# Kernel tuning notes

Measured on AMD Instinct MI355X. Metric: run time of the kernel, lower is better.

The kernel has to match this reference:

```python
import jax, jax.numpy as jnp
import numpy as np

EPS = 1e-8  # torch F.cosine_similarity norm clamp


def setup_inputs() -> dict:
    key = jax.random.key(0)
    k1, k2, k3, k4, k5 = jax.random.split(key, 5)
    C, S, H = 20000, 32, 256
    Cs = S // 2  # compressed_seq_len = int(S * 0.5)
    B = 64
    return {
        "query": jax.random.normal(k1, (B, H), dtype=jnp.float32),
        "episodes": jax.random.normal(k2, (C, S, H), dtype=jnp.float32),
        "compressed_episodes": jax.random.normal(k3, (C, Cs, H), dtype=jnp.float32),
        "episode_embeddings": jax.random.normal(k4, (C, H), dtype=jnp.float32),
        "is_compressed": jax.random.randint(k5, (C,), 0, 2) > 0,
        "k": 8,
    }


def reference(query, episodes, compressed_episodes, episode_embeddings, is_compressed, k):
    # Cosine similarity with torch-style eps clamping of each norm.
    qn = query / jnp.maximum(jnp.linalg.norm(query, axis=-1, keepdims=True), EPS)
    en = episode_embeddings / jnp.maximum(
        jnp.linalg.norm(episode_embeddings, axis=-1, keepdims=True), EPS
    )
    sims = qn @ en.T  # [B, C]

    top_scores, top_idx = jax.lax.top_k(sims, k)  # [B, k]

    B = query.shape[0]
    S, H = episodes.shape[1], episodes.shape[2]
    Cs = compressed_episodes.shape[1]

    full = episodes[top_idx]                 # [B, k, S, H] gather
    comp = compressed_episodes[top_idx]      # [B, k, Cs, H] gather
    pad = jnp.zeros((B, k, S - Cs, H), dtype=comp.dtype)
    padded = jnp.concatenate([comp, pad], axis=2)  # [B, k, S, H]

    mask = is_compressed[top_idx][:, :, None, None]  # [B, k, 1, 1]
    retrieved = jnp.where(mask, padded, full)        # [B, k, S, H]
    return retrieved, top_scores
```

## Files before the change

### kernel.cpp

```cpp
#include <hip/hip_runtime.h>
#include <math.h>

#define HDIM 256
#define H4   64
#define EPSN 1e-8f
#define CT   128
#define KC   8
#define NCH  8
#define QSTR 264

typedef unsigned long long u64;
typedef unsigned int       u32;
typedef __attribute__((ext_vector_type(8))) __bf16 bf16x8;
typedef __attribute__((ext_vector_type(4))) __bf16 bf16x4;
typedef __attribute__((ext_vector_type(4))) float  f32x4;

__device__ __forceinline__ u64 make_key(float v, int idx) {
    u32 u = __float_as_uint(v);
    u ^= (u & 0x80000000u) ? 0xFFFFFFFFu : 0x80000000u;
    return ((u64)u << 32) | (u32)(~idx);
}
__device__ __forceinline__ float key_val(u64 k) {
    u32 u = (u32)(k >> 32);
    u ^= (u & 0x80000000u) ? 0x80000000u : 0xFFFFFFFFu;
    return __uint_as_float(u);
}
__device__ __forceinline__ int key_idx(u64 k) { return (int)(~(u32)k); }

__device__ __forceinline__ void insert8(u64* ls, u64 k) {
    if (k > ls[7]) {
        ls[7] = k;
        #pragma unroll
        for (int j = 7; j > 0; --j)
            if (ls[j] > ls[j-1]) { u64 tmp = ls[j]; ls[j] = ls[j-1]; ls[j-1] = tmp; }
    }
}

__global__ __launch_bounds__(512)
void sims_kernel(const float4* __restrict__ q4, const float4* __restrict__ emb4,
                 const u32* __restrict__ mask4, u64* __restrict__ cand,
                 int* __restrict__ flags, int C, int B, int NT) {
    const int t = threadIdx.x;

    if (blockIdx.x == (unsigned)NT) {
        __shared__ int red0[8], red1[8];
        int lo = 0, lg = 0;
        const int n4 = C >> 2;
        int i = t;
        for (; i + 1536 < n4; i += 2048) {
            u32 v0 = mask4[i], v1 = mask4[i + 512], v2 = mask4[i + 1024], v3 = mask4[i + 1536];
            u32 o = v0 | v1 | v2 | v3;
            if (o & 0xFFFFFF00u) lo = 1;
            if (o & 0xFEFEFEFEu) lg = 1;
        }
        for (; i < n4; i += 512) {
            u32 v = mask4[i];
            if (v & 0xFFFFFF00u) lo = 1;
            if (v & 0xFEFEFEFEu) lg = 1;
        }
        const unsigned char* mb = (const unsigned char*)mask4;
        for (int j = (n4 << 2) + t; j < C; j += 512) {
            unsigned char v = mb[j];
            if (v > 1) lg = 1;
            if ((j & 3) != 0 && v != 0) lo = 1;
        }
        lo = __any(lo); lg = __any(lg);
        if ((t & 63) == 0) { red0[t >> 6] = lo; red1[t >> 6] = lg; }
        __syncthreads();
        if (t == 0) {
            int a0 = 0, a1 = 0;
            #pragma unroll
            for (int r = 0; r < 8; ++r) { a0 |= red0[r]; a1 |= red1[r]; }
            flags[0] = a0; flags[1] = a1;
        }
        return;
    }

    __shared__ union {
        struct { __bf16 qh[64][QSTR]; __bf16 ql[64][QSTR]; } st;
        struct { float sc[64][CT + 1]; u64 sp[64][7][8]; } ep;
    } sm;
    __shared__ float qn[64];
    __shared__ float en[CT];

    const int c0   = blockIdx.x * CT;
    const int lane = t & 63;
    const int w    = t >> 6;
    const int mrow = lane & 15;
    const int kg   = lane >> 4;
    const float4 z = make_float4(0.f, 0.f, 0.f, 0.f);

    const int  erow = c0 + w * 16 + mrow;
    const bool ev   = erow < C;
    const float4* erp = emb4 + (size_t)erow * H4 + kg * 2;
    float4 cur0 = ev ? erp[0] : z;
    float4 cur1 = ev ? erp[1] : z;
    float4 nxt0 = ev ? erp[KC]     : z;
    float4 nxt1 = ev ? erp[KC + 1] : z;

    {
        const int r  = t >> 3;
        const int c8 = (t & 7) * 8;
        float qp = 0.f;
        #pragma unroll
        for (int i = 0; i < 8; ++i) {
            float4 v = (r < B) ? q4[(size_t)r * H4 + c8 + i] : z;
            bf16x4 h, l;
            h.x = (__bf16)v.x; h.y = (__bf16)v.y; h.z = (__bf16)v.z; h.w = (__bf16)v.w;
            l.x = (__bf16)(v.x - (float)h.x); l.y = (__bf16)(v.y - (float)h.y);
            l.z = (__bf16)(v.z - (float)h.z); l.w = (__bf16)(v.w - (float)h.w);
            *(bf16x4*)&sm.st.qh[r][(c8 + i) * 4] = h;
            *(bf16x4*)&sm.st.ql[r][(c8 + i) * 4] = l;
            float x0 = (float)h.x + (float)l.x, x1 = (float)h.y + (float)l.y;
            float x2 = (float)h.z + (float)l.z, x3 = (float)h.w + (float)l.w;
            qp = fmaf(x0, x0, fmaf(x1, x1, fmaf(x2, x2, fmaf(x3, x3, qp))));
        }
        qp += __shfl_xor(qp, 1, 64);
        qp += __shfl_xor(qp, 2, 64);
        qp += __shfl_xor(qp, 4, 64);
        if ((t & 7) == 0) qn[r] = 1.f / fmaxf(sqrtf(qp), EPSN);
    }
    __syncthreads();

    f32x4 acc[4];
    #pragma unroll
    for (int m = 0; m < 4; ++m) acc[m] = (f32x4){0.f, 0.f, 0.f, 0.f};
    float epart = 0.f;

    #pragma unroll
    for (int ch = 0; ch < NCH; ++ch) {
        float4 n20 = z, n21 = z;
        if (ch + 2 < NCH) {
            n20 = ev ? erp[(ch + 2) * KC]     : z;
            n21 = ev ? erp[(ch + 2) * KC + 1] : z;
        }
        bf16x8 bh, bl;
        {
            float xs[8] = {cur0.x, cur0.y, cur0.z, cur0.w,
                           cur1.x, cur1.y, cur1.z, cur1.w};
            #pragma unroll
            for (int i = 0; i < 8; ++i) {
                __bf16 h = (__bf16)xs[i];
                __bf16 l = (__bf16)(xs[i] - (float)h);
                bh[i] = h; bl[i] = l;
                float x = (float)h + (float)l;
                epart = fmaf(x, x, epart);
            }
        }
        #pragma unroll
        for (int m = 0; m < 4; ++m) {
            bf16x8 ah = *(const bf16x8*)&sm.st.qh[m * 16 + mrow][ch * 32 + kg * 8];
            bf16x8 al = *(const bf16x8*)&sm.st.ql[m * 16 + mrow][ch * 32 + kg * 8];
            acc[m] = __builtin_amdgcn_mfma_f32_16x16x32_bf16(ah, bh, acc[m], 0, 0, 0);
            acc[m] = __builtin_amdgcn_mfma_f32_16x16x32_bf16(ah, bl, acc[m], 0, 0, 0);
            acc[m] = __builtin_amdgcn_mfma_f32_16x16x32_bf16(al, bh, acc[m], 0, 0, 0);
        }
        cur0 = nxt0; cur1 = nxt1;
        nxt0 = n20;  nxt1 = n21;
    }

    epart += __shfl_xor(epart, 16, 64);
    epart += __shfl_xor(epart, 32, 64);
    if (kg == 0) en[w * 16 + mrow] = 1.f / fmaxf(sqrtf(epart), EPSN);

    __syncthreads();

    const float ev2 = en[w * 16 + mrow];
    #pragma unroll
    for (int m = 0; m < 4; ++m) {
        #pragma unroll
        for (int r = 0; r < 4; ++r) {
            int b = m * 16 + kg * 4 + r;
            sm.ep.sc[b][w * 16 + mrow] = acc[m][r] * qn[b] * ev2;
        }
    }
    __syncthreads();

    const int sb = t & 63;
    const int g  = t >> 6;
    u64 ls[8];
    #pragma unroll
    for (int j = 0; j < 8; ++j) ls[j] = 0ull;
    #pragma unroll
    for (int i2 = 0; i2 < 16; ++i2) {
        int cl = g * 16 + i2;
        int c  = c0 + cl;
        if (c < C && sb < B) insert8(ls, make_key(sm.ep.sc[sb][cl], c));
    }
    if (g != 0) {
        #pragma unroll
        for (int r = 0; r < 8; ++r) sm.ep.sp[sb][g - 1][r] = ls[r];
    }
    __syncthreads();
    if (g == 0) {
        #pragma unroll
        for (int gg = 0; gg < 7; ++gg)
            #pragma unroll
            for (int r = 0; r < 8; ++r) insert8(ls, sm.ep.sp[sb][gg][r]);
        u64* dst = cand + (((size_t)blockIdx.x * 64) + sb) * 8;
        #pragma unroll
        for (int r = 0; r < 8; ++r) dst[r] = ls[r];
    }
}

__global__ __launch_bounds__(256)
void merge_kernel(const u64* __restrict__ cand,
                  float* __restrict__ scores_out, int* __restrict__ top_idx,
                  int B, int NT) {
    __shared__ u64 sh[256 * 8];
    const int b = blockIdx.x, t = threadIdx.x;

    u64 ls[8];
    #pragma unroll
    for (int j = 0; j < 8; ++j) ls[j] = 0ull;

    for (int tile = t; tile < NT; tile += 256) {
        const u64* pp = cand + (((size_t)tile * 64) + b) * 8;
        #pragma unroll
        for (int r = 0; r < 8; ++r) {
            u64 k = pp[r];
            if (k <= ls[7]) break;
            ls[7] = k;
            #pragma unroll
            for (int q = 7; q > 0; --q)
                if (ls[q] > ls[q-1]) { u64 tmp = ls[q]; ls[q] = ls[q-1]; ls[q-1] = tmp; }
        }
    }

    #pragma unroll
    for (int j = 0; j < 8; ++j) sh[t * 8 + j] = ls[j];
    __syncthreads();

    if (t < 64) {
        u64 m[8];
        #pragma unroll
        for (int j = 0; j < 8; ++j) m[j] = 0ull;
        for (int tt = 0; tt < 4; ++tt) {
            const u64* pp = &sh[(t * 4 + tt) * 8];
            #pragma unroll
            for (int j = 0; j < 8; ++j) {
                u64 k = pp[j];
                if (k <= m[7]) break;
                m[7] = k;
                #pragma unroll
                for (int q = 7; q > 0; --q)
                    if (m[q] > m[q-1]) { u64 tmp = m[q]; m[q] = m[q-1]; m[q-1] = tmp; }
            }
        }
        for (int r = 0; r < 8; ++r) {
            u64 best = m[0];
            #pragma unroll
            for (int off = 32; off; off >>= 1) {
                u64 o = __shfl_xor(best, off, 64);
                if (o > best) best = o;
            }
            if (m[0] == best) {
                #pragma unroll
                for (int q = 0; q < 7; ++q) m[q] = m[q+1];
                m[7] = 0ull;
            }
            if (t == 0) {
                scores_out[b * 8 + r] = key_val(best);
                top_idx[b * 8 + r]    = key_idx(best);
            }
        }
    }
}

__global__ __launch_bounds__(256)
void gather_kernel(const float* __restrict__ episodes,
                   const float* __restrict__ compressed,
                   const void* __restrict__ is_comp,
                   const int* __restrict__ top_idx,
                   const int* __restrict__ flags,
                   float* __restrict__ out,
                   int S, int Cs) {
    const int bj  = blockIdx.x >> 1;
    const int h   = blockIdx.x & 1;
    const int idx = top_idx[bj];
    const int f_off = flags[0], f_gt1 = flags[1];

    bool comp;
    if      (f_gt1) comp = ((const float*)is_comp)[idx] != 0.f;
    else if (f_off) comp = ((const unsigned char*)is_comp)[idx] != 0;
    else            comp = ((const int*)is_comp)[idx] != 0;

    const int n4   = S * H4;
    const int c4   = Cs * H4;
    const int half = n4 >> 1;
    const int v0   = h * half;

    const float4* full4 = (const float4*)episodes   + (size_t)idx * n4;
    const float4* cmp4  = (const float4*)compressed + (size_t)idx * c4;
    float4* out4 = (float4*)out + (size_t)bj * n4;
    const float4 z = make_float4(0.f, 0.f, 0.f, 0.f);

    if (comp) {
        #pragma unroll 4
        for (int v = v0 + threadIdx.x; v < v0 + half; v += 256)
            out4[v] = (v < c4) ? cmp4[v] : z;
    } else {
        #pragma unroll 4
        for (int v = v0 + threadIdx.x; v < v0 + half; v += 256)
            out4[v] = full4[v];
    }
}

extern "C" void kernel_launch(void* const* d_in, const int* in_sizes, int n_in,
                              void* d_out, int out_size, void* d_ws, size_t ws_size,
                              hipStream_t stream) {
    const float* query      = (const float*)d_in[0];
    const float* episodes   = (const float*)d_in[1];
    const float* compressed = (const float*)d_in[2];
    const float* emb        = (const float*)d_in[3];
    const void*  is_comp    = d_in[4];

    const int B  = in_sizes[0] / HDIM;
    const int C  = in_sizes[3] / HDIM;
    const int S  = in_sizes[1] / (C * HDIM);
    const int Cs = in_sizes[2] / (C * HDIM);
    const int K  = 8;
    const int NT = (C + CT - 1) / CT;

    float* out        = (float*)d_out;
    float* scores_out = out + (size_t)B * K * S * HDIM;

    u64*  cand    = (u64*)d_ws;
    int*  top_idx = (int*)(cand + (size_t)NT * 64 * 8);
    int*  flags   = top_idx + B * K;

    sims_kernel<<<NT + 1, 512, 0, stream>>>(
        (const float4*)query, (const float4*)emb, (const u32*)is_comp,
        cand, flags, C, B, NT);
    merge_kernel<<<B, 256, 0, stream>>>(cand, scores_out, top_idx, B, NT);
    gather_kernel<<<B * K * 2, 256, 0, stream>>>(episodes, compressed, is_comp,
                                                 top_idx, flags, out, S, Cs);
}
```

Before: 46.55 us.

## Fuse top-k merge into gather kernel, recomputing merge per gather block

```diff
diff --git a/kernel.cpp b/kernel.cpp
--- a/kernel.cpp
+++ b/kernel.cpp
@@ -204,18 +204,28 @@
 }
 
 __global__ __launch_bounds__(256)
-void merge_kernel(const u64* __restrict__ cand,
-                  float* __restrict__ scores_out, int* __restrict__ top_idx,
-                  int B, int NT) {
+void gather_kernel(const float* __restrict__ episodes,
+                   const float* __restrict__ compressed,
+                   const void* __restrict__ is_comp,
+                   const u64* __restrict__ cand,
+                   const int* __restrict__ flags,
+                   float* __restrict__ out,
+                   float* __restrict__ scores_out,
+                   int S, int Cs, int NT) {
     __shared__ u64 sh[256 * 8];
-    const int b = blockIdx.x, t = threadIdx.x;
+    __shared__ u64 kj_sh;
+
+    const int t  = threadIdx.x;
+    const int bj = blockIdx.x >> 1;
+    const int h  = blockIdx.x & 1;
+    const int b  = bj >> 3;
+    const int j  = bj & 7;
 
     u64 ls[8];
     #pragma unroll
-    for (int j = 0; j < 8; ++j) ls[j] = 0ull;
-
-    for (int tile = t; tile < NT; tile += 256) {
-        const u64* pp = cand + (((size_t)tile * 64) + b) * 8;
+    for (int r = 0; r < 8; ++r) ls[r] = 0ull;
+    if (t < NT) {
+        const u64* pp = cand + (((size_t)t * 64) + b) * 8;
         #pragma unroll
         for (int r = 0; r < 8; ++r) {
             u64 k = pp[r];
@@ -226,20 +236,19 @@
                 if (ls[q] > ls[q-1]) { u64 tmp = ls[q]; ls[q] = ls[q-1]; ls[q-1] = tmp; }
         }
     }
-
-    #pragma unroll
-    for (int j = 0; j < 8; ++j) sh[t * 8 + j] = ls[j];
+    #pragma unroll
+    for (int r = 0; r < 8; ++r) sh[t * 8 + r] = ls[r];
     __syncthreads();
 
     if (t < 64) {
         u64 m[8];
         #pragma unroll
-        for (int j = 0; j < 8; ++j) m[j] = 0ull;
+        for (int r = 0; r < 8; ++r) m[r] = 0ull;
         for (int tt = 0; tt < 4; ++tt) {
             const u64* pp = &sh[(t * 4 + tt) * 8];
             #pragma unroll
-            for (int j = 0; j < 8; ++j) {
-                u64 k = pp[j];
+            for (int r = 0; r < 8; ++r) {
+                u64 k = pp[r];
                 if (k <= m[7]) break;
                 m[7] = k;
                 #pragma unroll
@@ -247,7 +256,7 @@
                     if (m[q] > m[q-1]) { u64 tmp = m[q]; m[q] = m[q-1]; m[q-1] = tmp; }
             }
         }
-        for (int r = 0; r < 8; ++r) {
+        for (int r = 0; r <= j; ++r) {
             u64 best = m[0];
             #pragma unroll
             for (int off = 32; off; off >>= 1) {
@@ -259,27 +268,16 @@
                 for (int q = 0; q < 7; ++q) m[q] = m[q+1];
                 m[7] = 0ull;
             }
-            if (t == 0) {
-                scores_out[b * 8 + r] = key_val(best);
-                top_idx[b * 8 + r]    = key_idx(best);
-            }
-        }
-    }
-}
-
-__global__ __launch_bounds__(256)
-void gather_kernel(const float* __restrict__ episodes,
-                   const float* __restrict__ compressed,
-                   const void* __restrict__ is_comp,
-                   const int* __restrict__ top_idx,
-                   const int* __restrict__ flags,
-                   float* __restrict__ out,
-                   int S, int Cs) {
-    const int bj  = blockIdx.x >> 1;
-    const int h   = blockIdx.x & 1;
-    const int idx = top_idx[bj];
+            if (t == 0 && r == j) kj_sh = best;
+        }
+    }
+    __syncthreads();
+
+    const u64 kj  = kj_sh;
+    const int idx = key_idx(kj);
+    if (h == 0 && t == 0) scores_out[bj] = key_val(kj);
+
     const int f_off = flags[0], f_gt1 = flags[1];
-
     bool comp;
     if      (f_gt1) comp = ((const float*)is_comp)[idx] != 0.f;
     else if (f_off) comp = ((const unsigned char*)is_comp)[idx] != 0;
@@ -297,11 +295,11 @@
 
     if (comp) {
         #pragma unroll 4
-        for (int v = v0 + threadIdx.x; v < v0 + half; v += 256)
+        for (int v = v0 + t; v < v0 + half; v += 256)
             out4[v] = (v < c4) ? cmp4[v] : z;
     } else {
         #pragma unroll 4
-        for (int v = v0 + threadIdx.x; v < v0 + half; v += 256)
+        for (int v = v0 + t; v < v0 + half; v += 256)
             out4[v] = full4[v];
     }
 }
@@ -325,14 +323,13 @@
     float* out        = (float*)d_out;
     float* scores_out = out + (size_t)B * K * S * HDIM;
 
-    u64*  cand    = (u64*)d_ws;
-    int*  top_idx = (int*)(cand + (size_t)NT * 64 * 8);
-    int*  flags   = top_idx + B * K;
+    u64*  cand  = (u64*)d_ws;
+    int*  flags = (int*)(cand + (size_t)NT * 64 * 8);
 
     sims_kernel<<<NT + 1, 512, 0, stream>>>(
         (const float4*)query, (const float4*)emb, (const u32*)is_comp,
         cand, flags, C, B, NT);
-    merge_kernel<<<B, 256, 0, stream>>>(cand, scores_out, top_idx, B, NT);
     gather_kernel<<<B * K * 2, 256, 0, stream>>>(episodes, compressed, is_comp,
-                                                 top_idx, flags, out, S, Cs);
-}
+                                                 cand, flags, out, scores_out,
+                                                 S, Cs, NT);
+}
```

New measurement: 52.72 us. 1.13x slower.

## Fuse top-k merge into sims kernel via last-block atomic ticket

Applied to the files above, without the earlier changes.

```diff
diff --git a/kernel.cpp b/kernel.cpp
--- a/kernel.cpp
+++ b/kernel.cpp
@@ -39,7 +39,9 @@
 __global__ __launch_bounds__(512)
 void sims_kernel(const float4* __restrict__ q4, const float4* __restrict__ emb4,
                  const u32* __restrict__ mask4, u64* __restrict__ cand,
-                 int* __restrict__ flags, int C, int B, int NT) {
+                 int* __restrict__ flags, int* __restrict__ top_idx,
+                 float* __restrict__ scores_out, u32* __restrict__ ctr,
+                 int C, int B, int NT) {
     const int t = threadIdx.x;
 
     if (blockIdx.x == (unsigned)NT) {
@@ -82,6 +84,8 @@
     } sm;
     __shared__ float qn[64];
     __shared__ float en[CT];
+    __shared__ u64   mg[64][8][8];
+    __shared__ int   last_flag;
 
     const int c0   = blockIdx.x * CT;
     const int lane = t & 63;
@@ -201,68 +205,83 @@
         #pragma unroll
         for (int r = 0; r < 8; ++r) dst[r] = ls[r];
     }
-}
-
-__global__ __launch_bounds__(256)
-void merge_kernel(const u64* __restrict__ cand,
-                  float* __restrict__ scores_out, int* __restrict__ top_idx,
-                  int B, int NT) {
-    __shared__ u64 sh[256 * 8];
-    const int b = blockIdx.x, t = threadIdx.x;
-
-    u64 ls[8];
-    #pragma unroll
-    for (int j = 0; j < 8; ++j) ls[j] = 0ull;
-
-    for (int tile = t; tile < NT; tile += 256) {
-        const u64* pp = cand + (((size_t)tile * 64) + b) * 8;
-        #pragma unroll
-        for (int r = 0; r < 8; ++r) {
-            u64 k = pp[r];
-            if (k <= ls[7]) break;
-            ls[7] = k;
+
+    __threadfence();
+    __syncthreads();
+    if (t == 0) {
+        u32 ticket = __hip_atomic_fetch_add(ctr, 1u, __ATOMIC_ACQ_REL,
+                                            __HIP_MEMORY_SCOPE_AGENT);
+        last_flag = (ticket == (u32)(NT - 1));
+    }
+    __syncthreads();
+    if (!last_flag) return;
+
+    __threadfence();
+    {
+        const int mb2 = t >> 3;
+        const int mh  = t & 7;
+        u64 ms[8];
+        #pragma unroll
+        for (int r = 0; r < 8; ++r) ms[r] = 0ull;
+
+        #define PROCESS(tt, kf) do {                                          \
+            if ((kf) > ms[7]) {                                               \
+                const u64* rp = cand + (((size_t)(tt)) * 64 + mb2) * 8;       \
+                u64 kk = (kf);                                                \
+                int rr = 1;                                                   \
+                while (1) {                                                   \
+                    ms[7] = kk;                                               \
+                    _Pragma("unroll")                                         \
+                    for (int q = 7; q > 0; --q)                               \
+                        if (ms[q] > ms[q-1]) { u64 tm = ms[q]; ms[q] = ms[q-1]; ms[q-1] = tm; } \
+                    if (rr >= 8) break;                                       \
+                    kk = rp[rr++];                                            \
+                    if (kk <= ms[7]) break;                                   \
+                }                                                             \
+            }                                                                 \
+        } while (0)
+
+        int tile = mh;
+        for (; tile + 24 < NT; tile += 32) {
+            u64 k0 = cand[(((size_t)tile)      * 64 + mb2) * 8];
+            u64 k1 = cand[(((size_t)tile + 8)  * 64 + mb2) * 8];
+            u64 k2 = cand[(((size_t)tile + 16) * 64 + mb2) * 8];
+            u64 k3 = cand[(((size_t)tile + 24) * 64 + mb2) * 8];
+            PROCESS(tile,      k0);
+            PROCESS(tile + 8,  k1);
+            PROCESS(tile + 16, k2);
+            PROCESS(tile + 24, k3);
+        }
+        for (; tile < NT; tile += 8) {
+            u64 kf = cand[(((size_t)tile) * 64 + mb2) * 8];
+            PROCESS(tile, kf);
+        }
+        #undef PROCESS
+
+        #pragma unroll
+        for (int r = 0; r < 8; ++r) mg[mb2][mh][r] = ms[r];
+    }
+    __syncthreads();
+    if (t < 64) {
+        u64 fs[8];
+        #pragma unroll
+        for (int r = 0; r < 8; ++r) fs[r] = 0ull;
+        #pragma unroll
+        for (int hh = 0; hh < 8; ++hh) {
             #pragma unroll
-            for (int q = 7; q > 0; --q)
-                if (ls[q] > ls[q-1]) { u64 tmp = ls[q]; ls[q] = ls[q-1]; ls[q-1] = tmp; }
-        }
-    }
-
-    #pragma unroll
-    for (int j = 0; j < 8; ++j) sh[t * 8 + j] = ls[j];
-    __syncthreads();
-
-    if (t < 64) {
-        u64 m[8];
-        #pragma unroll
-        for (int j = 0; j < 8; ++j) m[j] = 0ull;
-        for (int tt = 0; tt < 4; ++tt) {
-            const u64* pp = &sh[(t * 4 + tt) * 8];
-            #pragma unroll
-            for (int j = 0; j < 8; ++j) {
-                u64 k = pp[j];
-                if (k <= m[7]) break;
-                m[7] = k;
+            for (int r = 0; r < 8; ++r) {
+                u64 k = mg[t][hh][r];
+                if (k <= fs[7]) break;
+                fs[7] = k;
                 #pragma unroll
                 for (int q = 7; q > 0; --q)
-                    if (m[q] > m[q-1]) { u64 tmp = m[q]; m[q] = m[q-1]; m[q-1] = tmp; }
+                    if (fs[q] > fs[q-1]) { u64 tm = fs[q]; fs[q] = fs[q-1]; fs[q-1] = tm; }
             }
         }
+        #pragma unroll
         for (int r = 0; r < 8; ++r) {
-            u64 best = m[0];
-            #pragma unroll
-            for (int off = 32; off; off >>= 1) {
-                u64 o = __shfl_xor(best, off, 64);
-                if (o > best) best = o;
-            }
-            if (m[0] == best) {
-                #pragma unroll
-                for (int q = 0; q < 7; ++q) m[q] = m[q+1];
-                m[7] = 0ull;
-            }
-            if (t == 0) {
-                scores_out[b * 8 + r] = key_val(best);
-                top_idx[b * 8 + r]    = key_idx(best);
-            }
+            scores_out[t * 8 + r] = key_val(fs[r]);
+            top_idx[t * 8 + r]    = key_idx(fs[r]);
         }
     }
 }
@@ -325,14 +344,15 @@
     float* out        = (float*)d_out;
     float* scores_out = out + (size_t)B * K * S * HDIM;
 
-    u64*  cand    = (u64*)d_ws;
-    int*  top_idx = (int*)(cand + (size_t)NT * 64 * 8);
-    int*  flags   = top_idx + B * K;
-
+    u32*  ctr     = (u32*)d_ws;
+    int*  flags   = (int*)((char*)d_ws + 16);
+    int*  top_idx = (int*)((char*)d_ws + 64);
+    u64*  cand    = (u64*)((char*)d_ws + 4096);
+
+    hipMemsetAsync(d_ws, 0, 16, stream);
     sims_kernel<<<NT + 1, 512, 0, stream>>>(
         (const float4*)query, (const float4*)emb, (const u32*)is_comp,
-        cand, flags, C, B, NT);
-    merge_kernel<<<B, 256, 0, stream>>>(cand, scores_out, top_idx, B, NT);
+        cand, flags, top_idx, scores_out, ctr, C, B, NT);
     gather_kernel<<<B * K * 2, 256, 0, stream>>>(episodes, compressed, is_comp,
                                                  top_idx, flags, out, S, Cs);
 }
```

After: 119.6 us. +157.0%, slower.
